# Kernel optimization log

Hardware: AMD Instinct MI355X
Metric: run time of the kernel (lower is better)

The kernel has to match this reference:

```python
import jax, jax.numpy as jnp
import numpy as np

INPUT_DIM = 1024
MEMORY_DIM = 512
MEMORY_SIZE = 4096
TOPK = 8


def setup_inputs() -> dict:
    key = jax.random.key(0)
    ks = jax.random.split(key, 7)
    query = jax.random.normal(ks[0], (8, 4096, INPUT_DIM), dtype=jnp.float32)
    memory_keys = jax.random.normal(ks[1], (MEMORY_SIZE, MEMORY_DIM), dtype=jnp.float32)
    memory_values = jax.random.normal(ks[2], (MEMORY_SIZE, MEMORY_DIM), dtype=jnp.float32)
    # nn.Linear-style init (uniform +-1/sqrt(fan_in))
    wq = jax.random.uniform(ks[3], (INPUT_DIM, MEMORY_DIM), jnp.float32, -1.0, 1.0) / np.sqrt(INPUT_DIM)
    bq = jax.random.uniform(ks[4], (MEMORY_DIM,), jnp.float32, -1.0, 1.0) / np.sqrt(INPUT_DIM)
    wo = jax.random.uniform(ks[5], (MEMORY_DIM, INPUT_DIM), jnp.float32, -1.0, 1.0) / np.sqrt(MEMORY_DIM)
    bo = jax.random.uniform(ks[6], (INPUT_DIM,), jnp.float32, -1.0, 1.0) / np.sqrt(MEMORY_DIM)
    return {"query": query, "memory_keys": memory_keys, "memory_values": memory_values,
            "wq": wq, "bq": bq, "wo": wo, "bo": bo}


def reference(query, memory_keys, memory_values, wq, bq, wo, bo):
    B, S, D = query.shape
    # Query projection: [B,S,M]
    q = jnp.einsum('bsd,dm->bsm', query, wq) + bq
    # Scores vs memory keys: [B,S,memory_size] (no expand needed)
    scores = jnp.einsum('bsm,km->bsk', q, memory_keys)
    # Top-k selection + softmax over selected scores
    topk_w, topk_idx = jax.lax.top_k(scores, TOPK)           # [B,S,K]
    topk_w = jax.nn.softmax(topk_w, axis=-1)
    # Gather selected memory values: [B,S,K,M]
    top_vals = memory_values[topk_idx]
    mem_out = jnp.einsum('bskm,bsk->bsm', top_vals, topk_w)  # weighted sum
    out = jnp.einsum('bsm,md->bsd', mem_out, wo) + bo
    return out + query
```

## Files before the change

### kernel.cpp

```cpp
#include <hip/hip_runtime.h>
#include <cstdint>

typedef _Float16 f16;
typedef uint32_t u32;
typedef f16 f16x2 __attribute__((ext_vector_type(2)));
typedef f16 f16x8 __attribute__((ext_vector_type(8)));
typedef float f32x4 __attribute__((ext_vector_type(4)));
typedef float f32x16 __attribute__((ext_vector_type(16)));
typedef u32 u32x4 __attribute__((ext_vector_type(4)));

#define NROWS 32768
#define D_IN 1024
#define M_DIM 512
#define NKEYS 4096
#define KTOP 8

__device__ __forceinline__ u32 umax32(u32 a, u32 b) { return a > b ? a : b; }
__device__ __forceinline__ u32 umin32(u32 a, u32 b) { return a < b ? a : b; }

__device__ __forceinline__ void gload_lds16(const void* src, void* dst) {
  __builtin_amdgcn_global_load_lds(
      (const __attribute__((address_space(1))) uint32_t*)src,
      (__attribute__((address_space(3))) uint32_t*)dst, 16, 0, 0);
}

__global__ void prep_kernel(const float* __restrict__ keys, const float* __restrict__ values,
                            const float* __restrict__ wq, const float* __restrict__ wo,
                            f16* __restrict__ keys_h, f16* __restrict__ values_h,
                            f16* __restrict__ wqT, f16* __restrict__ woT) {
  const int b = blockIdx.x, t = threadIdx.x;
  if (b < 2048) {
    const float* src = (b < 1024) ? keys : values;
    f16* dst = (b < 1024) ? keys_h : values_h;
    const int bb = b & 1023;
    const size_t base = (size_t)bb * 2048 + (size_t)t * 8;
    f32x4 a = *(const f32x4*)(src + base);
    f32x4 c2 = *(const f32x4*)(src + base + 4);
    f16x8 o;
    o[0] = (f16)a[0]; o[1] = (f16)a[1]; o[2] = (f16)a[2]; o[3] = (f16)a[3];
    o[4] = (f16)c2[0]; o[5] = (f16)c2[1]; o[6] = (f16)c2[2]; o[7] = (f16)c2[3];
    *(f16x8*)(dst + base) = o;
    return;
  }
  __shared__ float lds[64][65];
  if (b < 2176) {
    const int tb = b - 2048;
    const int td = tb >> 3, tm = tb & 7;
#pragma unroll
    for (int p = 0; p < 16; ++p) {
      const int d_loc = p * 4 + (t >> 6), m_loc = t & 63;
      lds[d_loc][m_loc] = wq[(size_t)(td * 64 + d_loc) * 512 + tm * 64 + m_loc];
    }
    __syncthreads();
#pragma unroll
    for (int p = 0; p < 16; ++p) {
      const int m_loc = p * 4 + (t >> 6), d_loc = t & 63;
      wqT[(size_t)(tm * 64 + m_loc) * 1024 + td * 64 + d_loc] = (f16)lds[d_loc][m_loc];
    }
  } else {
    const int tb = b - 2176;
    const int tmm = tb >> 4, tod = tb & 15;
#pragma unroll
    for (int p = 0; p < 16; ++p) {
      const int m_loc = p * 4 + (t >> 6), od_loc = t & 63;
      lds[m_loc][od_loc] = wo[(size_t)(tmm * 64 + m_loc) * 1024 + tod * 64 + od_loc];
    }
    __syncthreads();
#pragma unroll
    for (int p = 0; p < 16; ++p) {
      const int od_loc = p * 4 + (t >> 6), m_loc = t & 63;
      woT[(size_t)(tod * 64 + od_loc) * 512 + tmm * 64 + m_loc] = (f16)lds[m_loc][od_loc];
    }
  }
}

__global__ __launch_bounds__(256, 2) void qproj_kernel(
    const float* __restrict__ query, const f16* __restrict__ wqT,
    const float* __restrict__ bq, f16* __restrict__ q_out) {
  __shared__ f16 Atile[32 * 1024];
  const int tid = threadIdx.x;
  const int wave = tid >> 6, lane = tid & 63;
  const int g = lane >> 4, c = lane & 15;
  const int rowbase = blockIdx.x * 64 + wave * 16;
  const int row = rowbase + c;

  f16x8 Breg[32];
  {
    const float* qrow = query + (size_t)row * D_IN;
#pragma unroll
    for (int kk = 0; kk < 32; ++kk) {
      f32x4 lo = *(const f32x4*)(qrow + kk * 32 + g * 8);
      f32x4 hi = *(const f32x4*)(qrow + kk * 32 + g * 8 + 4);
      f16x8 v;
      v[0] = (f16)lo[0]; v[1] = (f16)lo[1]; v[2] = (f16)lo[2]; v[3] = (f16)lo[3];
      v[4] = (f16)hi[0]; v[5] = (f16)hi[1]; v[6] = (f16)hi[2]; v[7] = (f16)hi[3];
      Breg[kk] = v;
    }
  }

  for (int mt = 0; mt < 16; ++mt) {
    __syncthreads();
#pragma unroll
    for (int i2 = 0; i2 < 8; ++i2) {
      const int kr = wave * 8 + i2;
#pragma unroll
      for (int hb = 0; hb < 2; ++hb) {
        const u32 slot = (u32)(hb * 1024 + lane * 16);
        const u32 kb = slot ^ (u32)((kr & 7) << 4);
        const char* src = (const char*)(wqT + (size_t)(mt * 32 + kr) * D_IN) + kb;
        gload_lds16(src, (char*)Atile + kr * 2048 + hb * 1024);
      }
    }
    asm volatile("s_waitcnt vmcnt(0)" ::: "memory");
    __syncthreads();

    f32x4 acc0 = {0.f, 0.f, 0.f, 0.f};
    f32x4 acc1 = {0.f, 0.f, 0.f, 0.f};
#pragma unroll
    for (int kk = 0; kk < 32; ++kk) {
      const u32 base = (u32)(kk * 64 + g * 16);
      {
        const int ml = c;
        const u32 off = (u32)(ml * 2048) + (base ^ (u32)((ml & 7) << 4));
        f16x8 a = *(const f16x8*)((const char*)Atile + off);
        acc0 = __builtin_amdgcn_mfma_f32_16x16x32_f16(a, Breg[kk], acc0, 0, 0, 0);
      }
      {
        const int ml = 16 + c;
        const u32 off = (u32)(ml * 2048) + (base ^ (u32)((ml & 7) << 4));
        f16x8 a = *(const f16x8*)((const char*)Atile + off);
        acc1 = __builtin_amdgcn_mfma_f32_16x16x32_f16(a, Breg[kk], acc1, 0, 0, 0);
      }
    }

    f32x4 bq0 = *(const f32x4*)(bq + mt * 32 + g * 4);
    f32x4 bq1 = *(const f32x4*)(bq + mt * 32 + 16 + g * 4);
    f16* qp = q_out + (size_t)row * M_DIM + mt * 32 + g * 4;
    f16x2 p;
    p[0] = (f16)(acc0[0] + bq0[0]); p[1] = (f16)(acc0[1] + bq0[1]); *(f16x2*)(qp + 0) = p;
    p[0] = (f16)(acc0[2] + bq0[2]); p[1] = (f16)(acc0[3] + bq0[3]); *(f16x2*)(qp + 2) = p;
    p[0] = (f16)(acc1[0] + bq1[0]); p[1] = (f16)(acc1[1] + bq1[1]); *(f16x2*)(qp + 16) = p;
    p[0] = (f16)(acc1[2] + bq1[2]); p[1] = (f16)(acc1[3] + bq1[3]); *(f16x2*)(qp + 18) = p;
  }
}

__global__ __launch_bounds__(256, 2) void scores_topk_kernel(
    const f16* __restrict__ q, const f16* __restrict__ keys_h,
    u32* __restrict__ cand) {
  __shared__ f16 Ktile[2 * 32 * 512];
  const int tid = threadIdx.x;
  const int wave = tid >> 6, lane = tid & 63;
  const int h = lane >> 5, r32 = lane & 31;
  const int rb = blockIdx.x >> 1, half = blockIdx.x & 1;
  const int rowbase = rb * 128 + wave * 32;
  const int myrow = rowbase + r32;
  const int keybase = half * 2048;

  f16x8 Breg[32];
  {
    const f16* qr = q + (size_t)myrow * M_DIM;
#pragma unroll
    for (int kk = 0; kk < 32; ++kk)
      Breg[kk] = *(const f16x8*)(qr + kk * 16 + h * 8);
  }

  u32 topE[KTOP], topO[KTOP];
#pragma unroll
  for (int j = 0; j < KTOP; ++j) { topE[j] = 0u; topO[j] = 0u; }

  const int laneoff = r32 * M_DIM + h * 8;
  auto stage = [&](int buf, int kt) {
    const f16* tsrc = keys_h + (size_t)(keybase + kt * 32) * M_DIM + laneoff;
    char* dbase = (char*)Ktile + buf * 32768 + wave * 8192;
#pragma unroll
    for (int i2 = 0; i2 < 8; ++i2) {
      const int kk = wave * 8 + i2;
      gload_lds16(tsrc + kk * 16, dbase + i2 * 1024);
    }
  };

  const char* base_rd = (const char*)Ktile + lane * 16;

  stage(0, 0);
  asm volatile("s_waitcnt vmcnt(0)" ::: "memory");
  __syncthreads();

  for (int kt = 0; kt < 64; ++kt) {
    const int cur = kt & 1;
    if (kt < 63) stage(cur ^ 1, kt + 1);

    f32x16 accA, accB;
#pragma unroll
    for (int i = 0; i < 16; ++i) { accA[i] = 0.f; accB[i] = 0.f; }
    const char* tb = base_rd + cur * 32768;
    __builtin_amdgcn_s_setprio(1);
#pragma unroll
    for (int kk = 0; kk < 32; kk += 2) {
      f16x8 fA = *(const f16x8*)(tb + kk * 1024);
      f16x8 fB = *(const f16x8*)(tb + (kk + 1) * 1024);
      accA = __builtin_amdgcn_mfma_f32_32x32x16_f16(fA, Breg[kk], accA, 0, 0, 0);
      accB = __builtin_amdgcn_mfma_f32_32x32x16_f16(fB, Breg[kk + 1], accB, 0, 0, 0);
    }
    __builtin_amdgcn_s_setprio(0);

#pragma unroll
    for (int i = 0; i < 16; ++i) {
      const float s = accA[i] + accB[i];
      const u32 kidx = (u32)(keybase + kt * 32 + (i & 3) + 8 * (i >> 2) + 4 * h);
      const int bi = __float_as_int(s);
      const u32 mono = (u32)bi ^ (u32)((bi >> 31) | 0x80000000);
      u32 x = ((mono + 0x800u) & 0xFFFFF000u) | kidx;
      if ((i & 1) == 0) {
#pragma unroll
        for (int j = 0; j < KTOP; ++j) { const u32 nt = umax32(topE[j], x); x = umin32(topE[j], x); topE[j] = nt; }
      } else {
#pragma unroll
        for (int j = 0; j < KTOP; ++j) { const u32 nt = umax32(topO[j], x); x = umin32(topO[j], x); topO[j] = nt; }
      }
    }

    asm volatile("s_waitcnt vmcnt(0)" ::: "memory");
    __syncthreads();
  }

#pragma unroll
  for (int j = 0; j < KTOP; ++j) {
    u32 x = topO[j];
#pragma unroll
    for (int jj = 0; jj < KTOP; ++jj) { const u32 nt = umax32(topE[jj], x); x = umin32(topE[jj], x); topE[jj] = nt; }
  }
  u32 oth[KTOP];
#pragma unroll
  for (int j = 0; j < KTOP; ++j) oth[j] = (u32)__shfl((int)topE[j], lane ^ 32);
#pragma unroll
  for (int j = 0; j < KTOP; ++j) {
    u32 x = oth[j];
#pragma unroll
    for (int jj = 0; jj < KTOP; ++jj) { const u32 nt = umax32(topE[jj], x); x = umin32(topE[jj], x); topE[jj] = nt; }
  }

  if (h == 0) {
    u32* cp = cand + (size_t)myrow * 16 + half * 8;
    u32x4 a, b;
    a.x = topE[0]; a.y = topE[1]; a.z = topE[2]; a.w = topE[3];
    b.x = topE[4]; b.y = topE[5]; b.z = topE[6]; b.w = topE[7];
    *(u32x4*)(cp) = a;
    *(u32x4*)(cp + 4) = b;
  }
}

__global__ __launch_bounds__(256, 4) void merge_gather_kernel(
    const u32* __restrict__ cand, const f16* __restrict__ values_h,
    f16* __restrict__ mem_out) {
  const int tid = threadIdx.x;
  const int wave = tid >> 6, lane = tid & 63;
  const int rowbase = blockIdx.x * 32 + wave * 8;
  const int myrow = rowbase + (lane & 7);

  const u32* cp = cand + (size_t)myrow * 16;
  u32x4 a0 = *(const u32x4*)(cp);
  u32x4 a1 = *(const u32x4*)(cp + 4);
  u32x4 b0 = *(const u32x4*)(cp + 8);
  u32x4 b1 = *(const u32x4*)(cp + 12);
  u32 top[KTOP] = {a0.x, a0.y, a0.z, a0.w, a1.x, a1.y, a1.z, a1.w};
  u32 ins[KTOP] = {b0.x, b0.y, b0.z, b0.w, b1.x, b1.y, b1.z, b1.w};
#pragma unroll
  for (int j = 0; j < KTOP; ++j) {
    u32 x = ins[j];
#pragma unroll
    for (int jj = 0; jj < KTOP; ++jj) { const u32 nt = umax32(top[jj], x); x = umin32(top[jj], x); top[jj] = nt; }
  }

  float w[KTOP]; u32 idx[KTOP];
  {
    float s[KTOP];
#pragma unroll
    for (int j = 0; j < KTOP; ++j) {
      const u32 mono = top[j] & 0xFFFFF000u;
      const u32 bits = (mono & 0x80000000u) ? (mono ^ 0x80000000u) : ~mono;
      s[j] = __int_as_float(bits);
      idx[j] = top[j] & 0xFFFu;
    }
    const float m0 = s[0];
    float sum = 0.f;
#pragma unroll
    for (int j = 0; j < KTOP; ++j) { w[j] = __expf(s[j] - m0); sum += w[j]; }
    const float inv = 1.f / sum;
#pragma unroll
    for (int j = 0; j < KTOP; ++j) w[j] *= inv;
  }

  for (int r = 0; r < 8; ++r) {
    float acc2[8];
#pragma unroll
    for (int e = 0; e < 8; ++e) acc2[e] = 0.f;
#pragma unroll
    for (int j = 0; j < KTOP; ++j) {
      const u32 ix = (u32)__shfl((int)idx[j], r);
      const float wj = __shfl(w[j], r);
      const f16x8 v = *(const f16x8*)(values_h + (size_t)ix * M_DIM + lane * 8);
#pragma unroll
      for (int e = 0; e < 8; ++e) acc2[e] += wj * (float)v[e];
    }
    f16x8 o;
#pragma unroll
    for (int e = 0; e < 8; ++e) o[e] = (f16)acc2[e];
    *(f16x8*)(mem_out + (size_t)(rowbase + r) * M_DIM + lane * 8) = o;
  }
}

__global__ __launch_bounds__(256, 2) void outproj_kernel(
    const f16* __restrict__ mem_h, const f16* __restrict__ woT,
    const float* __restrict__ bo, const float* __restrict__ query,
    float* __restrict__ out) {
  __shared__ f16 Atile[32 * 512];
  const int tid = threadIdx.x;
  const int wave = tid >> 6, lane = tid & 63;
  const int g = lane >> 4, c = lane & 15;
  const int rowbase = blockIdx.x * 64 + wave * 16;
  const int row = rowbase + c;

  f16x8 Breg[16];
  {
    const f16* mr = mem_h + (size_t)row * M_DIM;
#pragma unroll
    for (int kk = 0; kk < 16; ++kk)
      Breg[kk] = *(const f16x8*)(mr + kk * 32 + g * 8);
  }

  for (int mt = 0; mt < 32; ++mt) {
    __syncthreads();
#pragma unroll
    for (int i2 = 0; i2 < 8; ++i2) {
      const int kr = wave * 8 + i2;
      const u32 kb = ((u32)(lane * 16)) ^ ((u32)((kr & 7) << 4));
      const char* src = (const char*)(woT + (size_t)(mt * 32 + kr) * M_DIM) + kb;
      gload_lds16(src, (char*)Atile + kr * 1024);
    }
    asm volatile("s_waitcnt vmcnt(0)" ::: "memory");
    __syncthreads();

    f32x4 acc0 = {0.f, 0.f, 0.f, 0.f};
    f32x4 acc1 = {0.f, 0.f, 0.f, 0.f};
#pragma unroll
    for (int kk = 0; kk < 16; ++kk) {
      const u32 base = (u32)(kk * 64 + g * 16);
      {
        const int ml = c;
        const u32 off = (u32)(ml * 1024) + (base ^ (u32)((ml & 7) << 4));
        f16x8 a = *(const f16x8*)((const char*)Atile + off);
        acc0 = __builtin_amdgcn_mfma_f32_16x16x32_f16(a, Breg[kk], acc0, 0, 0, 0);
      }
      {
        const int ml = 16 + c;
        const u32 off = (u32)(ml * 1024) + (base ^ (u32)((ml & 7) << 4));
        f16x8 a = *(const f16x8*)((const char*)Atile + off);
        acc1 = __builtin_amdgcn_mfma_f32_16x16x32_f16(a, Breg[kk], acc1, 0, 0, 0);
      }
    }

    const int od0 = mt * 32 + g * 4;
    f32x4 bo0 = *(const f32x4*)(bo + od0);
    f32x4 bo1 = *(const f32x4*)(bo + od0 + 16);
    const float* qp = query + (size_t)row * D_IN + od0;
    f32x4 q0 = *(const f32x4*)(qp);
    f32x4 q1 = *(const f32x4*)(qp + 16);
    f32x4 o0, o1;
#pragma unroll
    for (int i = 0; i < 4; ++i) {
      o0[i] = acc0[i] + bo0[i] + q0[i];
      o1[i] = acc1[i] + bo1[i] + q1[i];
    }
    float* op = out + (size_t)row * D_IN + od0;
    *(f32x4*)(op) = o0;
    *(f32x4*)(op + 16) = o1;
  }
}

extern "C" void kernel_launch(void* const* d_in, const int* in_sizes, int n_in,
                              void* d_out, int out_size, void* d_ws, size_t ws_size,
                              hipStream_t stream) {
  (void)in_sizes; (void)n_in; (void)out_size;
  const float* query = (const float*)d_in[0];
  const float* mkeys = (const float*)d_in[1];
  const float* mvals = (const float*)d_in[2];
  const float* wq    = (const float*)d_in[3];
  const float* bq    = (const float*)d_in[4];
  const float* wo    = (const float*)d_in[5];
  const float* bo    = (const float*)d_in[6];
  float* out = (float*)d_out;

  char* ws = (char*)d_ws;
  f16* keys_h   = (f16*)(ws);
  f16* values_h = (f16*)(ws + (4u << 20));
  f16* wqT      = (f16*)(ws + (8u << 20));
  f16* woT      = (f16*)(ws + (9u << 20));
  f16* q_h      = (f16*)(ws + (10u << 20));
  f16* mem_h    = (f16*)(ws + (10u << 20) + (size_t)NROWS * M_DIM * 2);
  u32* cand     = (u32*)(ws + (10u << 20) + 2ull * (size_t)NROWS * M_DIM * 2);
  const size_t need = (10u << 20) + 2ull * (size_t)NROWS * M_DIM * 2
                    + (size_t)NROWS * 16 * 4;
  if (ws_size < need) return;

  prep_kernel<<<2304, 256, 0, stream>>>(mkeys, mvals, wq, wo, keys_h, values_h, wqT, woT);
  qproj_kernel<<<NROWS / 64, 256, 0, stream>>>(query, wqT, bq, q_h);
  scores_topk_kernel<<<(NROWS / 128) * 2, 256, 0, stream>>>(q_h, keys_h, cand);
  merge_gather_kernel<<<NROWS / 32, 256, 0, stream>>>(cand, values_h, mem_h);
  outproj_kernel<<<NROWS / 64, 256, 0, stream>>>(mem_h, woT, bo, query, out);
}
```

Before: 377.4 us.

## Split scores reduction dimension across wave pairs with LDS partial-sum exchange

The scores/top-k kernel now runs 512 threads per block. Each pair of waves splits the 512-wide reduction dimension in half, and the two waves exchange partial accumulators through LDS. Each wave then runs the top-k insertion on only half of the 32 keys per tile, which halves per-wave register use (Breg) and the sorting work, and raises occupancy. The cost is an extra block-wide barrier per key tile, LDS exchange traffic, and a final cross-wave merge of the two top-k lists.

```diff
diff --git a/kernel.cpp b/kernel.cpp
--- a/kernel.cpp
+++ b/kernel.cpp
@@ -144,23 +144,25 @@
   }
 }
 
-__global__ __launch_bounds__(256, 2) void scores_topk_kernel(
+__global__ __launch_bounds__(512, 4) void scores_topk_kernel(
     const f16* __restrict__ q, const f16* __restrict__ keys_h,
     u32* __restrict__ cand) {
   __shared__ f16 Ktile[2 * 32 * 512];
+  __shared__ float xchg[4 * 2 * 2 * 256];
   const int tid = threadIdx.x;
   const int wave = tid >> 6, lane = tid & 63;
   const int h = lane >> 5, r32 = lane & 31;
+  const int pair = wave >> 1, kpar = wave & 1;
   const int rb = blockIdx.x >> 1, half = blockIdx.x & 1;
-  const int rowbase = rb * 128 + wave * 32;
+  const int rowbase = rb * 128 + pair * 32;
   const int myrow = rowbase + r32;
   const int keybase = half * 2048;
 
-  f16x8 Breg[32];
+  f16x8 Breg[16];
   {
-    const f16* qr = q + (size_t)myrow * M_DIM;
-#pragma unroll
-    for (int kk = 0; kk < 32; ++kk)
+    const f16* qr = q + (size_t)myrow * M_DIM + kpar * 256;
+#pragma unroll
+    for (int kk = 0; kk < 16; ++kk)
       Breg[kk] = *(const f16x8*)(qr + kk * 16 + h * 8);
   }
 
@@ -171,15 +173,16 @@
   const int laneoff = r32 * M_DIM + h * 8;
   auto stage = [&](int buf, int kt) {
     const f16* tsrc = keys_h + (size_t)(keybase + kt * 32) * M_DIM + laneoff;
-    char* dbase = (char*)Ktile + buf * 32768 + wave * 8192;
-#pragma unroll
-    for (int i2 = 0; i2 < 8; ++i2) {
-      const int kk = wave * 8 + i2;
-      gload_lds16(tsrc + kk * 16, dbase + i2 * 1024);
+    char* dbase = (char*)Ktile + buf * 32768 + wave * 4096;
+#pragma unroll
+    for (int i2 = 0; i2 < 4; ++i2) {
+      const int s = wave * 4 + i2;
+      gload_lds16(tsrc + s * 16, dbase + i2 * 1024);
     }
   };
 
-  const char* base_rd = (const char*)Ktile + lane * 16;
+  float* xbase = xchg + pair * 1024;
+  const char* base_rd = (const char*)Ktile + kpar * 16384 + lane * 16;
 
   stage(0, 0);
   asm volatile("s_waitcnt vmcnt(0)" ::: "memory");
@@ -189,37 +192,64 @@
     const int cur = kt & 1;
     if (kt < 63) stage(cur ^ 1, kt + 1);
 
-    f32x16 accA, accB;
-#pragma unroll
-    for (int i = 0; i < 16; ++i) { accA[i] = 0.f; accB[i] = 0.f; }
+    f32x16 acc;
+#pragma unroll
+    for (int i = 0; i < 16; ++i) acc[i] = 0.f;
     const char* tb = base_rd + cur * 32768;
     __builtin_amdgcn_s_setprio(1);
 #pragma unroll
-    for (int kk = 0; kk < 32; kk += 2) {
+    for (int kk = 0; kk < 16; ++kk) {
       f16x8 fA = *(const f16x8*)(tb + kk * 1024);
-      f16x8 fB = *(const f16x8*)(tb + (kk + 1) * 1024);
-      accA = __builtin_amdgcn_mfma_f32_32x32x16_f16(fA, Breg[kk], accA, 0, 0, 0);
-      accB = __builtin_amdgcn_mfma_f32_32x32x16_f16(fB, Breg[kk + 1], accB, 0, 0, 0);
+      acc = __builtin_amdgcn_mfma_f32_32x32x16_f16(fA, Breg[kk], acc, 0, 0, 0);
     }
     __builtin_amdgcn_s_setprio(0);
 
-#pragma unroll
-    for (int i = 0; i < 16; ++i) {
-      const float s = accA[i] + accB[i];
-      const u32 kidx = (u32)(keybase + kt * 32 + (i & 3) + 8 * (i >> 2) + 4 * h);
-      const int bi = __float_as_int(s);
-      const u32 mono = (u32)bi ^ (u32)((bi >> 31) | 0x80000000);
-      u32 x = ((mono + 0x800u) & 0xFFFFF000u) | kidx;
-      if ((i & 1) == 0) {
-#pragma unroll
-        for (int j = 0; j < KTOP; ++j) { const u32 nt = umax32(topE[j], x); x = umin32(topE[j], x); topE[j] = nt; }
+    if (kpar == 0) {
+      f32x4 w0 = {acc[8], acc[9], acc[10], acc[11]};
+      f32x4 w1 = {acc[12], acc[13], acc[14], acc[15]};
+      float* wp = xbase + lane * 4;
+      *(f32x4*)(wp) = w0; *(f32x4*)(wp + 256) = w1;
+    } else {
+      f32x4 w0 = {acc[0], acc[1], acc[2], acc[3]};
+      f32x4 w1 = {acc[4], acc[5], acc[6], acc[7]};
+      float* wp = xbase + 512 + lane * 4;
+      *(f32x4*)(wp) = w0; *(f32x4*)(wp + 256) = w1;
+    }
+    asm volatile("s_waitcnt vmcnt(0)" ::: "memory");
+    __syncthreads();
+
+    {
+      const float* rp = xbase + (kpar ^ 1) * 512 + lane * 4;
+      f32x4 p0 = *(const f32x4*)(rp);
+      f32x4 p1 = *(const f32x4*)(rp + 256);
+      float s8[8];
+      if (kpar == 0) {
+        s8[0] = acc[0] + p0[0]; s8[1] = acc[1] + p0[1];
+        s8[2] = acc[2] + p0[2]; s8[3] = acc[3] + p0[3];
+        s8[4] = acc[4] + p1[0]; s8[5] = acc[5] + p1[1];
+        s8[6] = acc[6] + p1[2]; s8[7] = acc[7] + p1[3];
       } else {
-#pragma unroll
-        for (int j = 0; j < KTOP; ++j) { const u32 nt = umax32(topO[j], x); x = umin32(topO[j], x); topO[j] = nt; }
-      }
-    }
-
-    asm volatile("s_waitcnt vmcnt(0)" ::: "memory");
+        s8[0] = acc[8] + p0[0];  s8[1] = acc[9] + p0[1];
+        s8[2] = acc[10] + p0[2]; s8[3] = acc[11] + p0[3];
+        s8[4] = acc[12] + p1[0]; s8[5] = acc[13] + p1[1];
+        s8[6] = acc[14] + p1[2]; s8[7] = acc[15] + p1[3];
+      }
+#pragma unroll
+      for (int i = 0; i < 8; ++i) {
+        const int reg = kpar * 8 + i;
+        const u32 kidx = (u32)(keybase + kt * 32 + (reg & 3) + 8 * (reg >> 2) + 4 * h);
+        const int bi = __float_as_int(s8[i]);
+        const u32 mono = (u32)bi ^ (u32)((bi >> 31) | 0x80000000);
+        u32 x = ((mono + 0x800u) & 0xFFFFF000u) | kidx;
+        if ((i & 1) == 0) {
+#pragma unroll
+          for (int j = 0; j < KTOP; ++j) { const u32 nt = umax32(topE[j], x); x = umin32(topE[j], x); topE[j] = nt; }
+        } else {
+#pragma unroll
+          for (int j = 0; j < KTOP; ++j) { const u32 nt = umax32(topO[j], x); x = umin32(topO[j], x); topO[j] = nt; }
+        }
+      }
+    }
     __syncthreads();
   }
 
@@ -229,23 +259,38 @@
 #pragma unroll
     for (int jj = 0; jj < KTOP; ++jj) { const u32 nt = umax32(topE[jj], x); x = umin32(topE[jj], x); topE[jj] = nt; }
   }
-  u32 oth[KTOP];
-#pragma unroll
-  for (int j = 0; j < KTOP; ++j) oth[j] = (u32)__shfl((int)topE[j], lane ^ 32);
-#pragma unroll
-  for (int j = 0; j < KTOP; ++j) {
-    u32 x = oth[j];
-#pragma unroll
-    for (int jj = 0; jj < KTOP; ++jj) { const u32 nt = umax32(topE[jj], x); x = umin32(topE[jj], x); topE[jj] = nt; }
-  }
-
-  if (h == 0) {
-    u32* cp = cand + (size_t)myrow * 16 + half * 8;
-    u32x4 a, b;
-    a.x = topE[0]; a.y = topE[1]; a.z = topE[2]; a.w = topE[3];
-    b.x = topE[4]; b.y = topE[5]; b.z = topE[6]; b.w = topE[7];
-    *(u32x4*)(cp) = a;
-    *(u32x4*)(cp + 4) = b;
+  {
+    u32 oth[KTOP];
+#pragma unroll
+    for (int j = 0; j < KTOP; ++j) oth[j] = (u32)__shfl((int)topE[j], lane ^ 32);
+#pragma unroll
+    for (int j = 0; j < KTOP; ++j) {
+      u32 x = oth[j];
+#pragma unroll
+      for (int jj = 0; jj < KTOP; ++jj) { const u32 nt = umax32(topE[jj], x); x = umin32(topE[jj], x); topE[jj] = nt; }
+    }
+  }
+  u32* xm = (u32*)xchg + pair * 512;
+  if (kpar == 1) {
+#pragma unroll
+    for (int j = 0; j < KTOP; ++j) xm[j * 64 + lane] = topE[j];
+  }
+  __syncthreads();
+  if (kpar == 0) {
+#pragma unroll
+    for (int j = 0; j < KTOP; ++j) {
+      u32 x = xm[j * 64 + lane];
+#pragma unroll
+      for (int jj = 0; jj < KTOP; ++jj) { const u32 nt = umax32(topE[jj], x); x = umin32(topE[jj], x); topE[jj] = nt; }
+    }
+    if (h == 0) {
+      u32* cp = cand + (size_t)myrow * 16 + half * 8;
+      u32x4 a, b;
+      a.x = topE[0]; a.y = topE[1]; a.z = topE[2]; a.w = topE[3];
+      b.x = topE[4]; b.y = topE[5]; b.z = topE[6]; b.w = topE[7];
+      *(u32x4*)(cp) = a;
+      *(u32x4*)(cp + 4) = b;
+    }
   }
 }
 
@@ -404,7 +449,7 @@
 
   prep_kernel<<<2304, 256, 0, stream>>>(mkeys, mvals, wq, wo, keys_h, values_h, wqT, woT);
   qproj_kernel<<<NROWS / 64, 256, 0, stream>>>(query, wqT, bq, q_h);
-  scores_topk_kernel<<<(NROWS / 128) * 2, 256, 0, stream>>>(q_h, keys_h, cand);
+  scores_topk_kernel<<<(NROWS / 128) * 2, 512, 0, stream>>>(q_h, keys_h, cand);
   merge_gather_kernel<<<NROWS / 32, 256, 0, stream>>>(cand, values_h, mem_h);
   outproj_kernel<<<NROWS / 64, 256, 0, stream>>>(mem_h, woT, bo, query, out);
 }
```

Measured after the change: 472.1 us. 1.25x slower.
